# Kernel optimization log

Measured on AMD Instinct MI355X. Metric: run time of the kernel, lower is better.

## Reference

```python
import jax, jax.numpy as jnp
import numpy as np

# XORChainModel.forward: state[0] = inputs[0]; state[i] = state[i-1] ^ inputs[i]
# i.e. a cumulative XOR (inclusive prefix scan with XOR) along the chain axis.
# XOR is associative, so we use jax.lax.associative_scan (log-depth parallel scan).

SEQ_LEN = 4096  # number of steps in the XOR chain (len(inputs) list in torch)
BITS = 8192     # self.bits: width of each bit vector


def setup_inputs() -> dict:
    key = jax.random.key(0)
    # inputs[i] is a 1-D bit vector of length BITS; stack the whole list into [S, BITS]
    inputs = jax.random.randint(key, (SEQ_LEN, BITS), 0, 2, dtype=jnp.int32)
    return {"inputs": inputs}


def reference(inputs):
    # outputs[i] = inputs[0] ^ inputs[1] ^ ... ^ inputs[i]
    # Equivalent to the torch module's list of per-step states, stacked on axis 0.
    return jax.lax.associative_scan(jnp.bitwise_xor, inputs, axis=0)
```

## Files before the change

kernel.cpp:

```cpp
#include <hip/hip_runtime.h>


#define S 4096
#define B4 2048
#define TPB 256
#define NCT 8
#define OUTER 64
#define NOUT (S / OUTER)
#define NBLK (NOUT * NCT)
#define NWORDS (NOUT * B4)
#define POISON 0xAAAAAAAAu

typedef unsigned int v4u __attribute__((ext_vector_type(4)));
typedef unsigned long long u64;

__device__ __forceinline__ bool valid(unsigned w) {
    return (w & 0x300u) == 0x100u;
}
__device__ __forceinline__ u64 repl(unsigned nib) {
    u64 m = nib;
    m |= m << 4; m |= m << 8; m |= m << 16; m |= m << 32;
    return m;
}

__global__ __launch_bounds__(TPB, 2) void xor_bitpack(
        const v4u* __restrict__ in, v4u* __restrict__ out,
        unsigned* __restrict__ ctl) {
    unsigned* agg = ctl + 64;
    unsigned* inc = agg + NWORDS;

    __shared__ unsigned sh_t;
    const int tid = threadIdx.x;
    if (tid == 0) sh_t = atomicAdd(&ctl[0], 1u) - POISON;
    __syncthreads();
    const unsigned t = sh_t;
    const int ct   = (int)(t & (NCT - 1));
    const int o    = (int)(t >> 3);
    const int colg = ct * TPB + tid;

    const v4u* p = in + (size_t)o * OUTER * B4 + colg;

    u64 q[4] = {0ull, 0ull, 0ull, 0ull};
#pragma unroll
    for (int b = 0; b < 8; ++b) {
        v4u v[8];
#pragma unroll
        for (int j = 0; j < 8; ++j) v[j] = p[(size_t)(b * 8 + j) * B4];
#pragma unroll
        for (int j = 0; j < 8; ++j) {
            const int r = b * 8 + j;
            unsigned n = (v[j].x & 1u) | ((v[j].y & 1u) << 1) |
                         ((v[j].z & 1u) << 2) | ((v[j].w & 1u) << 3);
            q[r >> 4] ^= (u64)n << (4 * (r & 15));
        }
    }

    u64 tt = q[0] ^ q[1] ^ q[2] ^ q[3];
    tt ^= tt >> 32; tt ^= tt >> 16; tt ^= tt >> 8; tt ^= tt >> 4;
    const unsigned myagg = (unsigned)tt & 0xFu;
    __hip_atomic_store(&agg[(size_t)o * B4 + colg], 0x100u | myagg,
                       __ATOMIC_RELAXED, __HIP_MEMORY_SCOPE_AGENT);

    unsigned ex = 0u;
    int k = o - 1;
    while (k >= 0) {
        unsigned iw = __hip_atomic_load(&inc[(size_t)k * B4 + colg],
                                        __ATOMIC_RELAXED,
                                        __HIP_MEMORY_SCOPE_AGENT);
        if (valid(iw)) { ex ^= (iw & 0xFu); break; }
        int n = (k + 1 < 16) ? (k + 1) : 16;
        unsigned a[16];
        for (int j = 0; j < n; ++j)
            a[j] = __hip_atomic_load(&agg[(size_t)(k - j) * B4 + colg],
                                     __ATOMIC_RELAXED,
                                     __HIP_MEMORY_SCOPE_AGENT);
        int consumed = 0;
        for (int j = 0; j < n; ++j) {
            if (valid(a[j])) { ex ^= (a[j] & 0xFu); ++consumed; }
            else break;
        }
        k -= consumed;
        if (consumed == 0) __builtin_amdgcn_s_sleep(1);
    }
    __hip_atomic_store(&inc[(size_t)o * B4 + colg], 0x100u | (ex ^ myagg),
                       __ATOMIC_RELAXED, __HIP_MEMORY_SCOPE_AGENT);

    unsigned carry = ex;
    v4u* qo = out + (size_t)o * OUTER * B4 + colg;
#pragma unroll
    for (int kk = 0; kk < 4; ++kk) {
        u64 x = q[kk];
        x ^= x << 4; x ^= x << 8; x ^= x << 16; x ^= x << 32;
        const u64 f = x ^ repl(carry);
        carry ^= (unsigned)(x >> 60) & 0xFu;
#pragma unroll
        for (int j = 0; j < 16; ++j) {
            const unsigned n = (unsigned)(f >> (4 * j)) & 0xFu;
            v4u ov = (v4u){n & 1u, (n >> 1) & 1u, (n >> 2) & 1u, (n >> 3) & 1u};
            __builtin_nontemporal_store(ov, &qo[(size_t)(kk * 16 + j) * B4]);
        }
    }
}

extern "C" void kernel_launch(void* const* d_in, const int* in_sizes, int n_in,
                              void* d_out, int out_size, void* d_ws, size_t ws_size,
                              hipStream_t stream) {
    const v4u* in = (const v4u*)d_in[0];
    v4u* out = (v4u*)d_out;
    unsigned* ctl = (unsigned*)d_ws;

    xor_bitpack<<<NBLK, TPB, 0, stream>>>(in, out, ctl);
}
```

Baseline: 233.0 us.

## Convert to persistent blocks pulling small 8-row tiles from a ticket counter

Result: slower. 271.2 us (+16.4%).

```diff
diff --git a/kernel.cpp b/kernel.cpp
--- a/kernel.cpp
+++ b/kernel.cpp
@@ -5,25 +5,20 @@
 #define B4 2048
 #define TPB 256
 #define NCT 8
-#define OUTER 64
+#define OUTER 8
 #define NOUT (S / OUTER)
-#define NBLK (NOUT * NCT)
+#define NTICK (NOUT * NCT)
+#define NBLK 1024
 #define NWORDS (NOUT * B4)
 #define POISON 0xAAAAAAAAu
 
 typedef unsigned int v4u __attribute__((ext_vector_type(4)));
-typedef unsigned long long u64;
 
 __device__ __forceinline__ bool valid(unsigned w) {
     return (w & 0x300u) == 0x100u;
 }
-__device__ __forceinline__ u64 repl(unsigned nib) {
-    u64 m = nib;
-    m |= m << 4; m |= m << 8; m |= m << 16; m |= m << 32;
-    return m;
-}
 
-__global__ __launch_bounds__(TPB, 2) void xor_bitpack(
+__global__ __launch_bounds__(TPB, 4) void xor_persist(
         const v4u* __restrict__ in, v4u* __restrict__ out,
         unsigned* __restrict__ ctl) {
     unsigned* agg = ctl + 64;
@@ -31,73 +26,71 @@
 
     __shared__ unsigned sh_t;
     const int tid = threadIdx.x;
-    if (tid == 0) sh_t = atomicAdd(&ctl[0], 1u) - POISON;
-    __syncthreads();
-    const unsigned t = sh_t;
-    const int ct   = (int)(t & (NCT - 1));
-    const int o    = (int)(t >> 3);
-    const int colg = ct * TPB + tid;
 
-    const v4u* p = in + (size_t)o * OUTER * B4 + colg;
+    for (;;) {
+        if (tid == 0) sh_t = atomicAdd(&ctl[0], 1u) - POISON;
+        __syncthreads();
+        const unsigned t = sh_t;
+        __syncthreads();
+        if (t >= NTICK) return;
 
-    u64 q[4] = {0ull, 0ull, 0ull, 0ull};
+        const int ct       = (int)(t & (NCT - 1u));
+        const unsigned o   = t >> 3;
+        const int colg     = ct * TPB + tid;
+
+        const v4u* p = in + (size_t)o * OUTER * B4 + colg;
+        v4u v[OUTER];
 #pragma unroll
-    for (int b = 0; b < 8; ++b) {
-        v4u v[8];
+        for (int j = 0; j < OUTER; ++j) v[j] = p[(size_t)j * B4];
+
+        unsigned q = 0u;
 #pragma unroll
-        for (int j = 0; j < 8; ++j) v[j] = p[(size_t)(b * 8 + j) * B4];
-#pragma unroll
-        for (int j = 0; j < 8; ++j) {
-            const int r = b * 8 + j;
+        for (int j = 0; j < OUTER; ++j) {
             unsigned n = (v[j].x & 1u) | ((v[j].y & 1u) << 1) |
                          ((v[j].z & 1u) << 2) | ((v[j].w & 1u) << 3);
-            q[r >> 4] ^= (u64)n << (4 * (r & 15));
+            q |= n << (4 * j);
         }
-    }
 
-    u64 tt = q[0] ^ q[1] ^ q[2] ^ q[3];
-    tt ^= tt >> 32; tt ^= tt >> 16; tt ^= tt >> 8; tt ^= tt >> 4;
-    const unsigned myagg = (unsigned)tt & 0xFu;
-    __hip_atomic_store(&agg[(size_t)o * B4 + colg], 0x100u | myagg,
-                       __ATOMIC_RELAXED, __HIP_MEMORY_SCOPE_AGENT);
+        unsigned a = q;
+        a ^= a >> 16; a ^= a >> 8; a ^= a >> 4;
+        const unsigned myagg = a & 0xFu;
+        __hip_atomic_store(&agg[(size_t)o * B4 + colg], 0x100u | myagg,
+                           __ATOMIC_RELAXED, __HIP_MEMORY_SCOPE_AGENT);
 
-    unsigned ex = 0u;
-    int k = o - 1;
-    while (k >= 0) {
-        unsigned iw = __hip_atomic_load(&inc[(size_t)k * B4 + colg],
-                                        __ATOMIC_RELAXED,
-                                        __HIP_MEMORY_SCOPE_AGENT);
-        if (valid(iw)) { ex ^= (iw & 0xFu); break; }
-        int n = (k + 1 < 16) ? (k + 1) : 16;
-        unsigned a[16];
-        for (int j = 0; j < n; ++j)
-            a[j] = __hip_atomic_load(&agg[(size_t)(k - j) * B4 + colg],
-                                     __ATOMIC_RELAXED,
-                                     __HIP_MEMORY_SCOPE_AGENT);
-        int consumed = 0;
-        for (int j = 0; j < n; ++j) {
-            if (valid(a[j])) { ex ^= (a[j] & 0xFu); ++consumed; }
-            else break;
+        unsigned ex = 0u;
+        int k = (int)o - 1;
+        while (k >= 0) {
+            unsigned iw = __hip_atomic_load(&inc[(size_t)k * B4 + colg],
+                                            __ATOMIC_RELAXED,
+                                            __HIP_MEMORY_SCOPE_AGENT);
+            if (valid(iw)) { ex ^= (iw & 0xFu); break; }
+            int n = (k + 1 < 16) ? (k + 1) : 16;
+            unsigned aw[16];
+            for (int j = 0; j < n; ++j)
+                aw[j] = __hip_atomic_load(&agg[(size_t)(k - j) * B4 + colg],
+                                          __ATOMIC_RELAXED,
+                                          __HIP_MEMORY_SCOPE_AGENT);
+            int consumed = 0;
+            for (int j = 0; j < n; ++j) {
+                if (valid(aw[j])) { ex ^= (aw[j] & 0xFu); ++consumed; }
+                else break;
+            }
+            k -= consumed;
+            if (consumed == 0) __builtin_amdgcn_s_sleep(1);
         }
-        k -= consumed;
-        if (consumed == 0) __builtin_amdgcn_s_sleep(1);
-    }
-    __hip_atomic_store(&inc[(size_t)o * B4 + colg], 0x100u | (ex ^ myagg),
-                       __ATOMIC_RELAXED, __HIP_MEMORY_SCOPE_AGENT);
+        __hip_atomic_store(&inc[(size_t)o * B4 + colg], 0x100u | (ex ^ myagg),
+                           __ATOMIC_RELAXED, __HIP_MEMORY_SCOPE_AGENT);
 
-    unsigned carry = ex;
-    v4u* qo = out + (size_t)o * OUTER * B4 + colg;
+        unsigned x = q;
+        x ^= x << 4; x ^= x << 8; x ^= x << 16;
+        const unsigned f = x ^ (ex * 0x11111111u);
+
+        v4u* qo = out + (size_t)o * OUTER * B4 + colg;
 #pragma unroll
-    for (int kk = 0; kk < 4; ++kk) {
-        u64 x = q[kk];
-        x ^= x << 4; x ^= x << 8; x ^= x << 16; x ^= x << 32;
-        const u64 f = x ^ repl(carry);
-        carry ^= (unsigned)(x >> 60) & 0xFu;
-#pragma unroll
-        for (int j = 0; j < 16; ++j) {
-            const unsigned n = (unsigned)(f >> (4 * j)) & 0xFu;
+        for (int j = 0; j < OUTER; ++j) {
+            const unsigned n = (f >> (4 * j)) & 0xFu;
             v4u ov = (v4u){n & 1u, (n >> 1) & 1u, (n >> 2) & 1u, (n >> 3) & 1u};
-            __builtin_nontemporal_store(ov, &qo[(size_t)(kk * 16 + j) * B4]);
+            __builtin_nontemporal_store(ov, &qo[(size_t)j * B4]);
         }
     }
 }
@@ -109,5 +102,5 @@
     v4u* out = (v4u*)d_out;
     unsigned* ctl = (unsigned*)d_ws;
 
-    xor_bitpack<<<NBLK, TPB, 0, stream>>>(in, out, ctl);
+    xor_persist<<<NBLK, TPB, 0, stream>>>(in, out, ctl);
 }
```

## Stream input rows through LDS with double-buffered global_load_lds DMA

Applied to the files above, without the earlier changes.

After: 237.2 us. No clear change (+1.8%).

```diff
diff --git a/kernel.cpp b/kernel.cpp
--- a/kernel.cpp
+++ b/kernel.cpp
@@ -1,18 +1,23 @@
 #include <hip/hip_runtime.h>
+#include <stdint.h>
 
 
 #define S 4096
 #define B4 2048
-#define TPB 256
-#define NCT 8
+#define TPB 512
+#define NCT (B4 / TPB)
 #define OUTER 64
 #define NOUT (S / OUTER)
 #define NBLK (NOUT * NCT)
 #define NWORDS (NOUT * B4)
 #define POISON 0xAAAAAAAAu
+#define STG 4
+#define NSTG (OUTER / STG)
 
 typedef unsigned int v4u __attribute__((ext_vector_type(4)));
 typedef unsigned long long u64;
+typedef const __attribute__((address_space(1))) v4u* gp1_t;
+typedef __attribute__((address_space(3))) v4u* lp3_t;
 
 __device__ __forceinline__ bool valid(unsigned w) {
     return (w & 0x300u) == 0x100u;
@@ -23,36 +28,49 @@
     return m;
 }
 
-__global__ __launch_bounds__(TPB, 2) void xor_bitpack(
+__global__ __launch_bounds__(TPB) void xor_ldsdma(
         const v4u* __restrict__ in, v4u* __restrict__ out,
         unsigned* __restrict__ ctl) {
     unsigned* agg = ctl + 64;
     unsigned* inc = agg + NWORDS;
 
-    __shared__ unsigned sh_t;
-    const int tid = threadIdx.x;
-    if (tid == 0) sh_t = atomicAdd(&ctl[0], 1u) - POISON;
-    __syncthreads();
-    const unsigned t = sh_t;
-    const int ct   = (int)(t & (NCT - 1));
-    const int o    = (int)(t >> 3);
-    const int colg = ct * TPB + tid;
+    __shared__ v4u sh[2][STG][TPB];
+
+    const int tid   = (int)threadIdx.x;
+    const int bid   = (int)blockIdx.x;
+    const int ct    = bid & (NCT - 1);
+    const int o     = bid >> 2;
+    const int colg  = ct * TPB + tid;
+    const int wbase = tid & ~63;
 
     const v4u* p = in + (size_t)o * OUTER * B4 + colg;
 
+    auto STAGE = [&](int srow, int buf) {
+#pragma unroll
+        for (int j = 0; j < STG; ++j)
+            __builtin_amdgcn_global_load_lds(
+                (gp1_t)(const void*)(p + (size_t)(srow + j) * B4),
+                (lp3_t)(void*)&sh[buf][j][wbase], 16, 0, 0);
+    };
+
     u64 q[4] = {0ull, 0ull, 0ull, 0ull};
+    STAGE(0, 0);
+    STAGE(STG, 1);
 #pragma unroll
-    for (int b = 0; b < 8; ++b) {
-        v4u v[8];
+    for (int s = 0; s < NSTG; ++s) {
+        if (s < NSTG - 1) asm volatile("s_waitcnt vmcnt(4)" ::: "memory");
+        else              asm volatile("s_waitcnt vmcnt(0)" ::: "memory");
+        const int buf = s & 1;
 #pragma unroll
-        for (int j = 0; j < 8; ++j) v[j] = p[(size_t)(b * 8 + j) * B4];
-#pragma unroll
-        for (int j = 0; j < 8; ++j) {
-            const int r = b * 8 + j;
-            unsigned n = (v[j].x & 1u) | ((v[j].y & 1u) << 1) |
-                         ((v[j].z & 1u) << 2) | ((v[j].w & 1u) << 3);
+        for (int j = 0; j < STG; ++j) {
+            v4u v = sh[buf][j][tid];
+            unsigned n = (v.x & 1u) | ((v.y & 1u) << 1) |
+                         ((v.z & 1u) << 2) | ((v.w & 1u) << 3);
+            const int r = s * STG + j;
             q[r >> 4] ^= (u64)n << (4 * (r & 15));
         }
+        asm volatile("s_waitcnt lgkmcnt(0)" ::: "memory");
+        if (s + 2 < NSTG) STAGE((s + 2) * STG, buf);
     }
 
     u64 tt = q[0] ^ q[1] ^ q[2] ^ q[3];
@@ -109,5 +127,5 @@
     v4u* out = (v4u*)d_out;
     unsigned* ctl = (unsigned*)d_ws;
 
-    xor_bitpack<<<NBLK, TPB, 0, stream>>>(in, out, ctl);
+    xor_ldsdma<<<NBLK, TPB, 0, stream>>>(in, out, ctl);
 }
```
